# Optimization experiments

Measured on AMD Instinct MI355X. Metric: run time of the kernel, lower is better.

## Reference

```python
import jax, jax.numpy as jnp
import numpy as np

NUM_ITEMS = 50000
EMB = 16
SLATE = 10
HID = 512
LAT = 64
RESP = 1024
BATCH = 256


def _linear_params(k, out_dim, in_dim):
    kw, kb = jax.random.split(k)
    s = 1.0 / np.sqrt(in_dim)
    W = jax.random.uniform(kw, (out_dim, in_dim), jnp.float32, -s, s)
    b = jax.random.uniform(kb, (out_dim,), jnp.float32, -s, s)
    return W, b


def setup_inputs() -> dict:
    key = jax.random.key(0)
    ks = jax.random.split(key, 10)
    user_repr = jax.random.randint(ks[0], (BATCH, NUM_ITEMS), 0, 2, dtype=jnp.int32)
    slate = jax.random.randint(ks[1], (BATCH, SLATE), 0, NUM_ITEMS, dtype=jnp.int32)
    response_encoded = jax.random.uniform(ks[2], (BATCH, RESP), jnp.float32)
    eps = jax.random.normal(ks[3], (BATCH, LAT), jnp.float32)
    emb = jax.random.normal(ks[4], (NUM_ITEMS, EMB), jnp.float32)
    in_enc = SLATE * EMB + EMB + RESP
    W_enc, b_enc = _linear_params(ks[5], HID, in_enc)
    W_mu, b_mu = _linear_params(ks[6], LAT, HID)
    W_lv, b_lv = _linear_params(ks[7], LAT, HID)
    in_dec = LAT + EMB + RESP
    W_d1, b_d1 = _linear_params(ks[8], HID, in_dec)
    W_d2, b_d2 = _linear_params(ks[9], SLATE * EMB, HID)
    return {"user_repr": user_repr, "slate": slate, "response_encoded": response_encoded,
            "eps": eps, "emb": emb, "W_enc": W_enc, "b_enc": b_enc,
            "W_mu": W_mu, "b_mu": b_mu, "W_lv": W_lv, "b_lv": b_lv,
            "W_d1": W_d1, "b_d1": b_d1, "W_d2": W_d2, "b_d2": b_d2}


def reference(user_repr, slate, response_encoded, eps, emb,
              W_enc, b_enc, W_mu, b_mu, W_lv, b_lv, W_d1, b_d1, W_d2, b_d2):
    # Ragged embedding-mean pooling over interacted items (vectorized segment mean):
    # mean of emb rows where user_repr==1  ==  (indicator @ emb) / count
    uf = user_repr.astype(jnp.float32)                       # [B, N]
    counts = jnp.sum(uf, axis=1, keepdims=True)              # [B, 1]
    user = (uf @ emb) / counts                               # [B, E]

    cond = jnp.concatenate([user, response_encoded], axis=1)  # [B, E+R]
    slate_emb = emb[slate]                                    # [B, K, E]
    slate_vec = slate_emb.reshape(-1, SLATE * EMB)            # [B, K*E]
    x = jnp.concatenate([slate_vec, cond], axis=1)

    # encoder
    h = jax.nn.relu(x @ W_enc.T + b_enc)
    z_mean = h @ W_mu.T + b_mu
    z_log_var = h @ W_lv.T + b_lv

    # reparameterized sample
    z = z_mean + eps * jnp.exp(0.5 * z_log_var)

    # decoder
    dz = jnp.concatenate([z, cond], axis=1)
    dh = jax.nn.relu(dz @ W_d1.T + b_d1)
    rx = jax.nn.relu(dh @ W_d2.T + b_d2)                      # [B, K*E]
    rx = rx.reshape(-1, SLATE, EMB)                           # [B, K, E]

    # scores vs all items, softmax over items
    logits = jnp.einsum('bkh,nh->bkn', rx, emb)               # [B, K, N]
    probs = jax.nn.softmax(logits, axis=2)
    recon_slate = jnp.argmax(probs, axis=2)                   # [B, K]
    recon_resp = jnp.take_along_axis(probs, slate[:, :, None], axis=2)[..., 0]  # [B, K]
    return z_mean, z_log_var, recon_slate, recon_resp
```

## Files before the change

### kernel.cpp

```cpp
#include <hip/hip_runtime.h>

#define NITEMS 50000
#define EMBD   16
#define NSLATE 10
#define HIDD   512
#define LATD   64
#define RESPD  1024
#define BATCH  256
#define NCHUNK 8
#define CHUNK  6250
#define PCHUNK 3125
#define LOG2E  1.44269504088896340736f
#define SHIFT  64.0f

#define OUT_ZM 0
#define OUT_ZLV 16384
#define OUT_RS 32768
#define OUT_RR 35328

#define WS_X    0
#define WS_DZ   307200
#define WS_P2   0
#define WS_PP   589824
#define WS_PART 589824
#define WS_RX   1114112
#define WS_SPS  1155072
#define WS_SPM  1175552
#define WS_SPA  1196032

__global__ __launch_bounds__(256) void pool_part(const int* __restrict__ u,
    const float* __restrict__ emb, float* __restrict__ pp) {
  int b = blockIdx.x, c = blockIdx.y, t = threadIdx.x;
  float acc[16];
  #pragma unroll
  for (int i = 0; i < 16; ++i) acc[i] = 0.0f;
  float cnt = 0.0f;
  const int* ub = u + (size_t)b * NITEMS;
  int n1 = c * PCHUNK + PCHUNK;
  for (int n = c * PCHUNK + t; n < n1; n += 256) {
    if (ub[n]) {
      const float4* e4 = (const float4*)(emb + (size_t)n * 16);
      float4 a = e4[0], bb = e4[1], cc = e4[2], dd = e4[3];
      acc[0] += a.x;  acc[1] += a.y;  acc[2] += a.z;  acc[3] += a.w;
      acc[4] += bb.x; acc[5] += bb.y; acc[6] += bb.z; acc[7] += bb.w;
      acc[8] += cc.x; acc[9] += cc.y; acc[10] += cc.z; acc[11] += cc.w;
      acc[12] += dd.x; acc[13] += dd.y; acc[14] += dd.z; acc[15] += dd.w;
      cnt += 1.0f;
    }
  }
  #pragma unroll
  for (int off = 32; off > 0; off >>= 1) {
    #pragma unroll
    for (int i = 0; i < 16; ++i) acc[i] += __shfl_down(acc[i], off);
    cnt += __shfl_down(cnt, off);
  }
  int lane = t & 63, wv = t >> 6;
  if (lane == 0) {
    float* dst = pp + ((size_t)(b * 16 + c) * 4 + wv) * 17;
    #pragma unroll
    for (int i = 0; i < 16; ++i) dst[i] = acc[i];
    dst[16] = cnt;
  }
}

__global__ __launch_bounds__(256) void build_x(const float* __restrict__ pp,
    const int* __restrict__ slate, const float* __restrict__ resp,
    const float* __restrict__ emb, float* __restrict__ x, float* __restrict__ dz) {
  __shared__ float fin[17];
  int b = blockIdx.x, t = threadIdx.x;
  if (t < 17) {
    float a = 0.f;
    const float* p = pp + (size_t)b * 64 * 17 + t;
    #pragma unroll
    for (int w = 0; w < 64; ++w) a += p[w * 17];
    fin[t] = a;
  }
  __syncthreads();
  float inv = 1.0f / fin[16];
  if (t < 16) {
    float uv = fin[t] * inv;
    x[b * 1200 + 160 + t] = uv;
    dz[b * 1104 + 64 + t] = uv;
  }
  if (t >= 32 && t < 192) {
    int i = t - 32;
    int k = i >> 4, e = i & 15;
    int it = slate[b * 10 + k];
    x[b * 1200 + i] = emb[(size_t)it * 16 + e];
  }
  for (int i = t; i < 1024; i += 256) {
    float r = resp[b * 1024 + i];
    x[b * 1200 + 176 + i] = r;
    dz[b * 1104 + 80 + i] = r;
  }
}

__global__ __launch_bounds__(256) void gemm64(const float* __restrict__ A,
    const float* __restrict__ B, float* __restrict__ P, int M, int N, int K, int kChunk) {
  __shared__ float As[16][68];
  __shared__ float Bs[16][68];
  int tid = threadIdx.x;
  int m0 = blockIdx.y * 64, n0 = blockIdx.x * 64;
  int ks = blockIdx.z * kChunk;
  int ke = ks + kChunk; if (ke > K) ke = K;
  int sr = tid >> 2;
  int sc = (tid & 3) * 4;
  int tx = tid & 15, ty = tid >> 4;
  float acc[4][4];
  #pragma unroll
  for (int i = 0; i < 4; ++i)
    #pragma unroll
    for (int j = 0; j < 4; ++j) acc[i][j] = 0.f;
  for (int k0 = ks; k0 < ke; k0 += 16) {
    float4 av = make_float4(0.f, 0.f, 0.f, 0.f);
    float4 bv = make_float4(0.f, 0.f, 0.f, 0.f);
    if (k0 + sc < ke)
      av = *(const float4*)(A + (size_t)(m0 + sr) * K + k0 + sc);
    if (k0 + sc < ke && n0 + sr < N)
      bv = *(const float4*)(B + (size_t)(n0 + sr) * K + k0 + sc);
    __syncthreads();
    As[sc][sr] = av.x; As[sc + 1][sr] = av.y; As[sc + 2][sr] = av.z; As[sc + 3][sr] = av.w;
    Bs[sc][sr] = bv.x; Bs[sc + 1][sr] = bv.y; Bs[sc + 2][sr] = bv.z; Bs[sc + 3][sr] = bv.w;
    __syncthreads();
    #pragma unroll
    for (int kk = 0; kk < 16; ++kk) {
      float4 a4 = *(const float4*)&As[kk][4 * ty];
      float4 b4 = *(const float4*)&Bs[kk][4 * tx];
      float a[4] = {a4.x, a4.y, a4.z, a4.w};
      float b[4] = {b4.x, b4.y, b4.z, b4.w};
      #pragma unroll
      for (int i = 0; i < 4; ++i)
        #pragma unroll
        for (int j = 0; j < 4; ++j) acc[i][j] = fmaf(a[i], b[j], acc[i][j]);
    }
  }
  float* Pz = P + (size_t)blockIdx.z * M * N;
  #pragma unroll
  for (int i = 0; i < 4; ++i) {
    int m = m0 + 4 * ty + i, n = n0 + 4 * tx;
    if (n < N)
      *(float4*)(Pz + (size_t)m * N + n) = make_float4(acc[i][0], acc[i][1], acc[i][2], acc[i][3]);
  }
}

__global__ __launch_bounds__(128) void mulv_z_kernel(const float* __restrict__ part,
    const float* __restrict__ benc,
    const float* __restrict__ Wmu, const float* __restrict__ bmu,
    const float* __restrict__ Wlv, const float* __restrict__ blv,
    const float* __restrict__ eps, float* __restrict__ out, float* __restrict__ dz) {
  __shared__ __align__(16) float hs[512];
  __shared__ float zms[64], zlvs[64];
  int b = blockIdx.x, t = threadIdx.x;
  for (int i = t; i < 512; i += 128) {
    float a = benc[i];
    #pragma unroll
    for (int s = 0; s < 4; ++s) a += part[(size_t)s * 131072 + b * 512 + i];
    hs[i] = fmaxf(a, 0.f);
  }
  __syncthreads();
  const float* Wr = (t < 64) ? (Wmu + (size_t)t * 512) : (Wlv + (size_t)(t - 64) * 512);
  float bias = (t < 64) ? bmu[t] : blv[t - 64];
  const float4* w4 = (const float4*)Wr;
  const float4* h4 = (const float4*)hs;
  float a0 = 0.f, a1 = 0.f, a2 = 0.f, a3 = 0.f;
  #pragma unroll 4
  for (int i = 0; i < 128; ++i) {
    float4 w = w4[i], hv = h4[i];
    a0 = fmaf(w.x, hv.x, a0); a1 = fmaf(w.y, hv.y, a1);
    a2 = fmaf(w.z, hv.z, a2); a3 = fmaf(w.w, hv.w, a3);
  }
  float acc = (a0 + a1) + (a2 + a3) + bias;
  if (t < 64) { out[OUT_ZM + b * 64 + t] = acc; zms[t] = acc; }
  else        { out[OUT_ZLV + b * 64 + (t - 64)] = acc; zlvs[t - 64] = acc; }
  __syncthreads();
  if (t < 64) {
    float zv = fmaf(eps[b * 64 + t], __builtin_amdgcn_exp2f(0.7213475204444817f * zlvs[t]), zms[t]);
    dz[b * 1104 + t] = zv;
  }
}

__global__ __launch_bounds__(256) void gemm_d2(const float* __restrict__ part,
    const float* __restrict__ bd1, const float* __restrict__ W, float* __restrict__ p2) {
  __shared__ float As[16][68];
  __shared__ float Bs[16][68];
  const int N = 160;
  int tid = threadIdx.x;
  int m0 = blockIdx.y * 64, n0 = blockIdx.x * 64;
  int ks = blockIdx.z * 64, ke = ks + 64;
  int sr = tid >> 2, sc = (tid & 3) * 4;
  int tx = tid & 15, ty = tid >> 4;
  float acc[4][4];
  #pragma unroll
  for (int i = 0; i < 4; ++i)
    #pragma unroll
    for (int j = 0; j < 4; ++j) acc[i][j] = 0.f;
  for (int k0 = ks; k0 < ke; k0 += 16) {
    int col = k0 + sc;
    const float* p = part + (size_t)(m0 + sr) * 512 + col;
    float4 a0 = *(const float4*)(p);
    float4 a1 = *(const float4*)(p + 131072);
    float4 a2 = *(const float4*)(p + 262144);
    float4 a3 = *(const float4*)(p + 393216);
    float4 bb = *(const float4*)(bd1 + col);
    float4 av;
    av.x = fmaxf(a0.x + a1.x + a2.x + a3.x + bb.x, 0.f);
    av.y = fmaxf(a0.y + a1.y + a2.y + a3.y + bb.y, 0.f);
    av.z = fmaxf(a0.z + a1.z + a2.z + a3.z + bb.z, 0.f);
    av.w = fmaxf(a0.w + a1.w + a2.w + a3.w + bb.w, 0.f);
    float4 bv = make_float4(0.f, 0.f, 0.f, 0.f);
    if (n0 + sr < N)
      bv = *(const float4*)(W + (size_t)(n0 + sr) * 512 + col);
    __syncthreads();
    As[sc][sr] = av.x; As[sc + 1][sr] = av.y; As[sc + 2][sr] = av.z; As[sc + 3][sr] = av.w;
    Bs[sc][sr] = bv.x; Bs[sc + 1][sr] = bv.y; Bs[sc + 2][sr] = bv.z; Bs[sc + 3][sr] = bv.w;
    __syncthreads();
    #pragma unroll
    for (int kk = 0; kk < 16; ++kk) {
      float4 a4 = *(const float4*)&As[kk][4 * ty];
      float4 b4 = *(const float4*)&Bs[kk][4 * tx];
      float a[4] = {a4.x, a4.y, a4.z, a4.w};
      float b[4] = {b4.x, b4.y, b4.z, b4.w};
      #pragma unroll
      for (int i = 0; i < 4; ++i)
        #pragma unroll
        for (int j = 0; j < 4; ++j) acc[i][j] = fmaf(a[i], b[j], acc[i][j]);
    }
  }
  float* Pz = p2 + (size_t)blockIdx.z * 40960;
  #pragma unroll
  for (int i = 0; i < 4; ++i) {
    int m = m0 + 4 * ty + i, n = n0 + 4 * tx;
    if (n < N)
      *(float4*)(Pz + (size_t)m * 160 + n) = make_float4(acc[i][0], acc[i][1], acc[i][2], acc[i][3]);
  }
}

__global__ __launch_bounds__(256, 2) void score_part(const float* __restrict__ p2,
    const float* __restrict__ bd2, const float* __restrict__ emb,
    float* __restrict__ rx, float* __restrict__ psg, float* __restrict__ pmg,
    int* __restrict__ pag) {
  __shared__ __align__(16) float rxs[160];
  __shared__ float wm[4][10], wsum[4][10];
  __shared__ int wa[4][10];
  int b = blockIdx.x, c = blockIdx.y, t = threadIdx.x;
  if (t < 160) {
    float a = bd2[t];
    #pragma unroll
    for (int z = 0; z < 8; ++z) a += p2[(size_t)z * 40960 + b * 160 + t];
    float v = fmaxf(a, 0.f) * LOG2E;
    rxs[t] = v;
    if (c == 0) rx[b * 160 + t] = v;
  }
  __syncthreads();
  float m[10], s[10];
  int am[10];
  #pragma unroll
  for (int k = 0; k < 10; ++k) { m[k] = -3.402823466e38f; s[k] = 0.f; am[k] = 0; }
  int nBase = c * CHUNK;
  const float4* ep = (const float4*)emb;
  #pragma unroll 1
  for (int j = 0; j < 12; ++j) {
    int n0 = nBase + j * 512 + t;
    float4 e[2][4];
    #pragma unroll
    for (int it = 0; it < 2; ++it) {
      const float4* p = ep + (size_t)(n0 + it * 256) * 4;
      e[it][0] = p[0]; e[it][1] = p[1]; e[it][2] = p[2]; e[it][3] = p[3];
    }
    #pragma unroll
    for (int k = 0; k < 10; ++k) {
      float4 r0 = *(const float4*)(rxs + k * 16);
      float4 r1 = *(const float4*)(rxs + k * 16 + 4);
      float4 r2 = *(const float4*)(rxs + k * 16 + 8);
      float4 r3 = *(const float4*)(rxs + k * 16 + 12);
      #pragma unroll
      for (int it = 0; it < 2; ++it) {
        float x0 = fmaf(e[it][0].x, r0.x, -SHIFT);
        float x1 = e[it][1].x * r1.x;
        float x2 = e[it][2].x * r2.x;
        float x3 = e[it][3].x * r3.x;
        x0 = fmaf(e[it][0].y, r0.y, x0);
        x1 = fmaf(e[it][1].y, r1.y, x1);
        x2 = fmaf(e[it][2].y, r2.y, x2);
        x3 = fmaf(e[it][3].y, r3.y, x3);
        x0 = fmaf(e[it][0].z, r0.z, x0);
        x1 = fmaf(e[it][1].z, r1.z, x1);
        x2 = fmaf(e[it][2].z, r2.z, x2);
        x3 = fmaf(e[it][3].z, r3.z, x3);
        x0 = fmaf(e[it][0].w, r0.w, x0);
        x1 = fmaf(e[it][1].w, r1.w, x1);
        x2 = fmaf(e[it][2].w, r2.w, x2);
        x3 = fmaf(e[it][3].w, r3.w, x3);
        float x = (x0 + x1) + (x2 + x3);
        s[k] += __builtin_amdgcn_exp2f(x);
        if (x > m[k]) { m[k] = x; am[k] = n0 + it * 256; }
      }
    }
  }
  if (t < CHUNK - 6144) {
    int n = nBase + 6144 + t;
    const float4* p = ep + (size_t)n * 4;
    float4 e0 = p[0], e1 = p[1], e2 = p[2], e3 = p[3];
    #pragma unroll
    for (int k = 0; k < 10; ++k) {
      const float4 r0 = *(const float4*)(rxs + k * 16);
      const float4 r1 = *(const float4*)(rxs + k * 16 + 4);
      const float4 r2 = *(const float4*)(rxs + k * 16 + 8);
      const float4 r3 = *(const float4*)(rxs + k * 16 + 12);
      float x0 = fmaf(e0.w, r0.w, fmaf(e0.z, r0.z, fmaf(e0.y, r0.y, fmaf(e0.x, r0.x, -SHIFT))));
      float x1 = fmaf(e1.w, r1.w, fmaf(e1.z, r1.z, fmaf(e1.y, r1.y, e1.x * r1.x)));
      float x2 = fmaf(e2.w, r2.w, fmaf(e2.z, r2.z, fmaf(e2.y, r2.y, e2.x * r2.x)));
      float x3 = fmaf(e3.w, r3.w, fmaf(e3.z, r3.z, fmaf(e3.y, r3.y, e3.x * r3.x)));
      float x = (x0 + x1) + (x2 + x3);
      s[k] += __builtin_amdgcn_exp2f(x);
      if (x > m[k]) { m[k] = x; am[k] = n; }
    }
  }
  #pragma unroll
  for (int off = 32; off > 0; off >>= 1) {
    #pragma unroll
    for (int k = 0; k < 10; ++k) {
      s[k] += __shfl_down(s[k], off);
      float om = __shfl_down(m[k], off);
      int oa = __shfl_down(am[k], off);
      bool take = (om > m[k]) || (om == m[k] && oa < am[k]);
      am[k] = take ? oa : am[k];
      m[k] = fmaxf(m[k], om);
    }
  }
  int lane = t & 63, wv = t >> 6;
  if (lane == 0) {
    #pragma unroll
    for (int k = 0; k < 10; ++k) { wm[wv][k] = m[k]; wsum[wv][k] = s[k]; wa[wv][k] = am[k]; }
  }
  __syncthreads();
  if (t < 10) {
    int k = t;
    float M = wm[0][k], S = wsum[0][k];
    int AM = wa[0][k];
    #pragma unroll
    for (int w = 1; w < 4; ++w) {
      float m2 = wm[w][k];
      int oa = wa[w][k];
      bool take = (m2 > M) || (m2 == M && oa < AM);
      AM = take ? oa : AM;
      M = fmaxf(M, m2);
      S += wsum[w][k];
    }
    int idx = (b * NCHUNK + c) * 10 + k;
    psg[idx] = S; pmg[idx] = M; pag[idx] = AM;
  }
}

__global__ __launch_bounds__(256) void score_final(const float* __restrict__ psg,
    const float* __restrict__ pmg, const int* __restrict__ pag,
    const float* __restrict__ rx, const float* __restrict__ emb,
    const int* __restrict__ slate, float* __restrict__ out) {
  int tid = blockIdx.x * 256 + threadIdx.x;
  if (tid >= BATCH * 10) return;
  int b = tid / 10, k = tid % 10;
  int base = b * NCHUNK * 10 + k;
  float S = 0.f, M = -3.402823466e38f;
  int AM = 2147483647;
  #pragma unroll
  for (int c = 0; c < NCHUNK; ++c) {
    S += psg[base + c * 10];
    float m2 = pmg[base + c * 10];
    int oa = pag[base + c * 10];
    bool take = (m2 > M) || (m2 == M && oa < AM);
    AM = take ? oa : AM;
    M = fmaxf(M, m2);
  }
  int it = slate[b * 10 + k];
  const float* er = emb + (size_t)it * 16;
  const float* rr = rx + b * 160 + k * 16;
  float xs = -SHIFT;
  #pragma unroll
  for (int e = 0; e < 16; ++e) xs = fmaf(rr[e], er[e], xs);
  out[OUT_RS + b * 10 + k] = (float)AM;
  out[OUT_RR + b * 10 + k] = __builtin_amdgcn_exp2f(xs) / S;
}

extern "C" void kernel_launch(void* const* d_in, const int* in_sizes, int n_in,
                              void* d_out, int out_size, void* d_ws, size_t ws_size,
                              hipStream_t stream) {
  const int* user_repr = (const int*)d_in[0];
  const int* slate = (const int*)d_in[1];
  const float* resp = (const float*)d_in[2];
  const float* eps = (const float*)d_in[3];
  const float* emb = (const float*)d_in[4];
  const float* W_enc = (const float*)d_in[5];
  const float* b_enc = (const float*)d_in[6];
  const float* W_mu = (const float*)d_in[7];
  const float* b_mu = (const float*)d_in[8];
  const float* W_lv = (const float*)d_in[9];
  const float* b_lv = (const float*)d_in[10];
  const float* W_d1 = (const float*)d_in[11];
  const float* b_d1 = (const float*)d_in[12];
  const float* W_d2 = (const float*)d_in[13];
  const float* b_d2 = (const float*)d_in[14];
  float* out = (float*)d_out;
  float* ws = (float*)d_ws;

  float* x    = ws + WS_X;
  float* dz   = ws + WS_DZ;
  float* p2   = ws + WS_P2;
  float* pp   = ws + WS_PP;
  float* part = ws + WS_PART;
  float* rx   = ws + WS_RX;
  float* sps  = ws + WS_SPS;
  float* spm  = ws + WS_SPM;
  int*   spa  = (int*)(ws + WS_SPA);

  pool_part<<<dim3(256, 16), 256, 0, stream>>>(user_repr, emb, pp);
  build_x<<<256, 256, 0, stream>>>(pp, slate, resp, emb, x, dz);
  gemm64<<<dim3(8, 4, 4), 256, 0, stream>>>(x, W_enc, part, 256, 512, 1200, 300);
  mulv_z_kernel<<<256, 128, 0, stream>>>(part, b_enc, W_mu, b_mu, W_lv, b_lv, eps, out, dz);
  gemm64<<<dim3(8, 4, 4), 256, 0, stream>>>(dz, W_d1, part, 256, 512, 1104, 276);
  gemm_d2<<<dim3(3, 4, 8), 256, 0, stream>>>(part, b_d1, W_d2, p2);
  score_part<<<dim3(256, 8), 256, 0, stream>>>(p2, b_d2, emb, rx, sps, spm, spa);
  score_final<<<10, 256, 0, stream>>>(sps, spm, spa, rx, emb, slate, out);
}
```

Measured before the change: 323.5 us.

## Fuse d2 bias/ReLU into GEMM epilogue and prefetch embeddings in scoring loop

gemm_d2 no longer splits K into eight partial slices. It now runs the full K loop and applies bias, ReLU and the log2e scaling in its epilogue, writing rx directly. score_part then loads rx into registers instead of reducing partials through shared memory. The scoring loop is restructured to process one item per iteration with software prefetch of the next embedding row, which removes the tail branch. The gemm_d2 grid drops from 96 blocks to 12, so that GEMM loses parallelism, and score_part register pressure rises with 40 float4 values held in registers.

```diff
diff --git a/kernel.cpp b/kernel.cpp
--- a/kernel.cpp
+++ b/kernel.cpp
@@ -20,7 +20,6 @@
 
 #define WS_X    0
 #define WS_DZ   307200
-#define WS_P2   0
 #define WS_PP   589824
 #define WS_PART 589824
 #define WS_RX   1114112
@@ -180,13 +179,13 @@
 }
 
 __global__ __launch_bounds__(256) void gemm_d2(const float* __restrict__ part,
-    const float* __restrict__ bd1, const float* __restrict__ W, float* __restrict__ p2) {
+    const float* __restrict__ bd1, const float* __restrict__ W,
+    const float* __restrict__ bias, float* __restrict__ rx) {
   __shared__ float As[16][68];
   __shared__ float Bs[16][68];
-  const int N = 160;
+  const int N = 160, K = 512;
   int tid = threadIdx.x;
   int m0 = blockIdx.y * 64, n0 = blockIdx.x * 64;
-  int ks = blockIdx.z * 64, ke = ks + 64;
   int sr = tid >> 2, sc = (tid & 3) * 4;
   int tx = tid & 15, ty = tid >> 4;
   float acc[4][4];
@@ -194,7 +193,7 @@
   for (int i = 0; i < 4; ++i)
     #pragma unroll
     for (int j = 0; j < 4; ++j) acc[i][j] = 0.f;
-  for (int k0 = ks; k0 < ke; k0 += 16) {
+  for (int k0 = 0; k0 < K; k0 += 16) {
     int col = k0 + sc;
     const float* p = part + (size_t)(m0 + sr) * 512 + col;
     float4 a0 = *(const float4*)(p);
@@ -226,95 +225,75 @@
         for (int j = 0; j < 4; ++j) acc[i][j] = fmaf(a[i], b[j], acc[i][j]);
     }
   }
-  float* Pz = p2 + (size_t)blockIdx.z * 40960;
   #pragma unroll
   for (int i = 0; i < 4; ++i) {
     int m = m0 + 4 * ty + i, n = n0 + 4 * tx;
-    if (n < N)
-      *(float4*)(Pz + (size_t)m * 160 + n) = make_float4(acc[i][0], acc[i][1], acc[i][2], acc[i][3]);
-  }
-}
-
-__global__ __launch_bounds__(256, 2) void score_part(const float* __restrict__ p2,
-    const float* __restrict__ bd2, const float* __restrict__ emb,
-    float* __restrict__ rx, float* __restrict__ psg, float* __restrict__ pmg,
+    if (n < N) {
+      float4 v;
+      v.x = fmaxf(acc[i][0] + bias[n], 0.f) * LOG2E;
+      v.y = fmaxf(acc[i][1] + bias[n + 1], 0.f) * LOG2E;
+      v.z = fmaxf(acc[i][2] + bias[n + 2], 0.f) * LOG2E;
+      v.w = fmaxf(acc[i][3] + bias[n + 3], 0.f) * LOG2E;
+      *(float4*)(rx + (size_t)m * 160 + n) = v;
+    }
+  }
+}
+
+__global__ __launch_bounds__(256, 2) void score_part(const float* __restrict__ rx,
+    const float* __restrict__ emb, float* __restrict__ psg, float* __restrict__ pmg,
     int* __restrict__ pag) {
-  __shared__ __align__(16) float rxs[160];
   __shared__ float wm[4][10], wsum[4][10];
   __shared__ int wa[4][10];
   int b = blockIdx.x, c = blockIdx.y, t = threadIdx.x;
-  if (t < 160) {
-    float a = bd2[t];
-    #pragma unroll
-    for (int z = 0; z < 8; ++z) a += p2[(size_t)z * 40960 + b * 160 + t];
-    float v = fmaxf(a, 0.f) * LOG2E;
-    rxs[t] = v;
-    if (c == 0) rx[b * 160 + t] = v;
-  }
-  __syncthreads();
+  float4 r[10][4];
+  {
+    const float4* rp = (const float4*)(rx + b * 160);
+    #pragma unroll
+    for (int k = 0; k < 10; ++k) {
+      #pragma unroll
+      for (int j = 0; j < 4; ++j) r[k][j] = rp[k * 4 + j];
+    }
+  }
   float m[10], s[10];
   int am[10];
   #pragma unroll
   for (int k = 0; k < 10; ++k) { m[k] = -3.402823466e38f; s[k] = 0.f; am[k] = 0; }
-  int nBase = c * CHUNK;
+  int nBase = c * CHUNK, nEnd = nBase + CHUNK;
   const float4* ep = (const float4*)emb;
+  int n = nBase + t;
+  float4 e0, e1, e2, e3;
+  {
+    const float4* p = ep + (size_t)n * 4;
+    e0 = p[0]; e1 = p[1]; e2 = p[2]; e3 = p[3];
+  }
   #pragma unroll 1
-  for (int j = 0; j < 12; ++j) {
-    int n0 = nBase + j * 512 + t;
-    float4 e[2][4];
-    #pragma unroll
-    for (int it = 0; it < 2; ++it) {
-      const float4* p = ep + (size_t)(n0 + it * 256) * 4;
-      e[it][0] = p[0]; e[it][1] = p[1]; e[it][2] = p[2]; e[it][3] = p[3];
-    }
+  for (; n < nEnd; n += 256) {
+    int nn = n + 256; if (nn > NITEMS - 1) nn = NITEMS - 1;
+    const float4* p = ep + (size_t)nn * 4;
+    float4 f0 = p[0], f1 = p[1], f2 = p[2], f3 = p[3];
     #pragma unroll
     for (int k = 0; k < 10; ++k) {
-      float4 r0 = *(const float4*)(rxs + k * 16);
-      float4 r1 = *(const float4*)(rxs + k * 16 + 4);
-      float4 r2 = *(const float4*)(rxs + k * 16 + 8);
-      float4 r3 = *(const float4*)(rxs + k * 16 + 12);
-      #pragma unroll
-      for (int it = 0; it < 2; ++it) {
-        float x0 = fmaf(e[it][0].x, r0.x, -SHIFT);
-        float x1 = e[it][1].x * r1.x;
-        float x2 = e[it][2].x * r2.x;
-        float x3 = e[it][3].x * r3.x;
-        x0 = fmaf(e[it][0].y, r0.y, x0);
-        x1 = fmaf(e[it][1].y, r1.y, x1);
-        x2 = fmaf(e[it][2].y, r2.y, x2);
-        x3 = fmaf(e[it][3].y, r3.y, x3);
-        x0 = fmaf(e[it][0].z, r0.z, x0);
-        x1 = fmaf(e[it][1].z, r1.z, x1);
-        x2 = fmaf(e[it][2].z, r2.z, x2);
-        x3 = fmaf(e[it][3].z, r3.z, x3);
-        x0 = fmaf(e[it][0].w, r0.w, x0);
-        x1 = fmaf(e[it][1].w, r1.w, x1);
-        x2 = fmaf(e[it][2].w, r2.w, x2);
-        x3 = fmaf(e[it][3].w, r3.w, x3);
-        float x = (x0 + x1) + (x2 + x3);
-        s[k] += __builtin_amdgcn_exp2f(x);
-        if (x > m[k]) { m[k] = x; am[k] = n0 + it * 256; }
-      }
-    }
-  }
-  if (t < CHUNK - 6144) {
-    int n = nBase + 6144 + t;
-    const float4* p = ep + (size_t)n * 4;
-    float4 e0 = p[0], e1 = p[1], e2 = p[2], e3 = p[3];
-    #pragma unroll
-    for (int k = 0; k < 10; ++k) {
-      const float4 r0 = *(const float4*)(rxs + k * 16);
-      const float4 r1 = *(const float4*)(rxs + k * 16 + 4);
-      const float4 r2 = *(const float4*)(rxs + k * 16 + 8);
-      const float4 r3 = *(const float4*)(rxs + k * 16 + 12);
-      float x0 = fmaf(e0.w, r0.w, fmaf(e0.z, r0.z, fmaf(e0.y, r0.y, fmaf(e0.x, r0.x, -SHIFT))));
-      float x1 = fmaf(e1.w, r1.w, fmaf(e1.z, r1.z, fmaf(e1.y, r1.y, e1.x * r1.x)));
-      float x2 = fmaf(e2.w, r2.w, fmaf(e2.z, r2.z, fmaf(e2.y, r2.y, e2.x * r2.x)));
-      float x3 = fmaf(e3.w, r3.w, fmaf(e3.z, r3.z, fmaf(e3.y, r3.y, e3.x * r3.x)));
+      float x0 = fmaf(e0.x, r[k][0].x, -SHIFT);
+      float x1 = e1.x * r[k][1].x;
+      float x2 = e2.x * r[k][2].x;
+      float x3 = e3.x * r[k][3].x;
+      x0 = fmaf(e0.y, r[k][0].y, x0);
+      x1 = fmaf(e1.y, r[k][1].y, x1);
+      x2 = fmaf(e2.y, r[k][2].y, x2);
+      x3 = fmaf(e3.y, r[k][3].y, x3);
+      x0 = fmaf(e0.z, r[k][0].z, x0);
+      x1 = fmaf(e1.z, r[k][1].z, x1);
+      x2 = fmaf(e2.z, r[k][2].z, x2);
+      x3 = fmaf(e3.z, r[k][3].z, x3);
+      x0 = fmaf(e0.w, r[k][0].w, x0);
+      x1 = fmaf(e1.w, r[k][1].w, x1);
+      x2 = fmaf(e2.w, r[k][2].w, x2);
+      x3 = fmaf(e3.w, r[k][3].w, x3);
       float x = (x0 + x1) + (x2 + x3);
       s[k] += __builtin_amdgcn_exp2f(x);
       if (x > m[k]) { m[k] = x; am[k] = n; }
     }
+    e0 = f0; e1 = f1; e2 = f2; e3 = f3;
   }
   #pragma unroll
   for (int off = 32; off > 0; off >>= 1) {
@@ -404,7 +383,6 @@
 
   float* x    = ws + WS_X;
   float* dz   = ws + WS_DZ;
-  float* p2   = ws + WS_P2;
   float* pp   = ws + WS_PP;
   float* part = ws + WS_PART;
   float* rx   = ws + WS_RX;
@@ -417,7 +395,7 @@
   gemm64<<<dim3(8, 4, 4), 256, 0, stream>>>(x, W_enc, part, 256, 512, 1200, 300);
   mulv_z_kernel<<<256, 128, 0, stream>>>(part, b_enc, W_mu, b_mu, W_lv, b_lv, eps, out, dz);
   gemm64<<<dim3(8, 4, 4), 256, 0, stream>>>(dz, W_d1, part, 256, 512, 1104, 276);
-  gemm_d2<<<dim3(3, 4, 8), 256, 0, stream>>>(part, b_d1, W_d2, p2);
-  score_part<<<dim3(256, 8), 256, 0, stream>>>(p2, b_d2, emb, rx, sps, spm, spa);
+  gemm_d2<<<dim3(3, 4), 256, 0, stream>>>(part, b_d1, W_d2, b_d2, rx);
+  score_part<<<dim3(256, 8), 256, 0, stream>>>(rx, emb, sps, spm, spa);
   score_final<<<10, 256, 0, stream>>>(sps, spm, spa, rx, emb, slate, out);
 }
```

Result: slower. 352.5 us (+9.0%).

## Share staged embedding tiles across four batch rows in pooling kernel

Applied to the files above, without the earlier changes.

The pooling kernel now handles four batch rows per block. Each 256-item tile of the embedding table is staged once into padded shared memory and reused across all four rows, replacing per-row global gathers of embedding rows. This cuts redundant embedding reads and divergent gathers by a factor of four, but adds shared-memory staging, barriers and a larger register footprint (64 accumulators per thread). Grid size drops from 4096 to 1024 blocks.

```diff
diff --git a/kernel.cpp b/kernel.cpp
--- a/kernel.cpp
+++ b/kernel.cpp
@@ -10,6 +10,7 @@
 #define NCHUNK 8
 #define CHUNK  6250
 #define PCHUNK 3125
+#define PB     4
 #define LOG2E  1.44269504088896340736f
 #define SHIFT  64.0f
 
@@ -19,8 +20,8 @@
 #define OUT_RR 35328
 
 #define WS_X    0
+#define WS_P2   0
 #define WS_DZ   307200
-#define WS_P2   0
 #define WS_PP   589824
 #define WS_PART 589824
 #define WS_RX   1114112
@@ -30,36 +31,67 @@
 
 __global__ __launch_bounds__(256) void pool_part(const int* __restrict__ u,
     const float* __restrict__ emb, float* __restrict__ pp) {
-  int b = blockIdx.x, c = blockIdx.y, t = threadIdx.x;
-  float acc[16];
-  #pragma unroll
-  for (int i = 0; i < 16; ++i) acc[i] = 0.0f;
-  float cnt = 0.0f;
-  const int* ub = u + (size_t)b * NITEMS;
-  int n1 = c * PCHUNK + PCHUNK;
-  for (int n = c * PCHUNK + t; n < n1; n += 256) {
-    if (ub[n]) {
-      const float4* e4 = (const float4*)(emb + (size_t)n * 16);
-      float4 a = e4[0], bb = e4[1], cc = e4[2], dd = e4[3];
-      acc[0] += a.x;  acc[1] += a.y;  acc[2] += a.z;  acc[3] += a.w;
-      acc[4] += bb.x; acc[5] += bb.y; acc[6] += bb.z; acc[7] += bb.w;
-      acc[8] += cc.x; acc[9] += cc.y; acc[10] += cc.z; acc[11] += cc.w;
-      acc[12] += dd.x; acc[13] += dd.y; acc[14] += dd.z; acc[15] += dd.w;
-      cnt += 1.0f;
+  __shared__ float se[256 * 17];
+  int g = blockIdx.x, c = blockIdx.y, t = threadIdx.x;
+  int b0 = g * PB;
+  float acc[PB][16];
+  float cnt[PB];
+  #pragma unroll
+  for (int r = 0; r < PB; ++r) {
+    cnt[r] = 0.f;
+    #pragma unroll
+    for (int e = 0; e < 16; ++e) acc[r][e] = 0.f;
+  }
+  int base0 = c * PCHUNK;
+  const float4* emb4 = (const float4*)emb;
+  #pragma unroll 1
+  for (int st = 0; st < 13; ++st) {
+    int base = base0 + st * 256;
+    int tile = PCHUNK - st * 256; if (tile > 256) tile = 256;
+    int nf4 = tile * 4;
+    __syncthreads();
+    for (int v = t; v < nf4; v += 256) {
+      float4 f = emb4[(size_t)base * 4 + v];
+      int item = v >> 2, p = (v & 3) * 4;
+      se[item * 17 + p + 0] = f.x;
+      se[item * 17 + p + 1] = f.y;
+      se[item * 17 + p + 2] = f.z;
+      se[item * 17 + p + 3] = f.w;
+    }
+    __syncthreads();
+    if (t < tile) {
+      int n = base + t;
+      float ev[16];
+      #pragma unroll
+      for (int e = 0; e < 16; ++e) ev[e] = se[t * 17 + e];
+      #pragma unroll
+      for (int r = 0; r < PB; ++r) {
+        if (u[(size_t)(b0 + r) * NITEMS + n]) {
+          #pragma unroll
+          for (int e = 0; e < 16; ++e) acc[r][e] += ev[e];
+          cnt[r] += 1.f;
+        }
+      }
     }
   }
   #pragma unroll
   for (int off = 32; off > 0; off >>= 1) {
     #pragma unroll
-    for (int i = 0; i < 16; ++i) acc[i] += __shfl_down(acc[i], off);
-    cnt += __shfl_down(cnt, off);
+    for (int r = 0; r < PB; ++r) {
+      #pragma unroll
+      for (int e = 0; e < 16; ++e) acc[r][e] += __shfl_down(acc[r][e], off);
+      cnt[r] += __shfl_down(cnt[r], off);
+    }
   }
   int lane = t & 63, wv = t >> 6;
   if (lane == 0) {
-    float* dst = pp + ((size_t)(b * 16 + c) * 4 + wv) * 17;
-    #pragma unroll
-    for (int i = 0; i < 16; ++i) dst[i] = acc[i];
-    dst[16] = cnt;
+    #pragma unroll
+    for (int r = 0; r < PB; ++r) {
+      float* dst = pp + ((size_t)((b0 + r) * 16 + c) * 4 + wv) * 17;
+      #pragma unroll
+      for (int e = 0; e < 16; ++e) dst[e] = acc[r][e];
+      dst[16] = cnt[r];
+    }
   }
 }
 
@@ -103,8 +135,7 @@
   int m0 = blockIdx.y * 64, n0 = blockIdx.x * 64;
   int ks = blockIdx.z * kChunk;
   int ke = ks + kChunk; if (ke > K) ke = K;
-  int sr = tid >> 2;
-  int sc = (tid & 3) * 4;
+  int sr = tid >> 2, sc = (tid & 3) * 4;
   int tx = tid & 15, ty = tid >> 4;
   float acc[4][4];
   #pragma unroll
@@ -404,15 +435,15 @@
 
   float* x    = ws + WS_X;
   float* dz   = ws + WS_DZ;
-  float* p2   = ws + WS_P2;
   float* pp   = ws + WS_PP;
   float* part = ws + WS_PART;
+  float* p2   = ws + WS_P2;
   float* rx   = ws + WS_RX;
   float* sps  = ws + WS_SPS;
   float* spm  = ws + WS_SPM;
   int*   spa  = (int*)(ws + WS_SPA);
 
-  pool_part<<<dim3(256, 16), 256, 0, stream>>>(user_repr, emb, pp);
+  pool_part<<<dim3(64, 16), 256, 0, stream>>>(user_repr, emb, pp);
   build_x<<<256, 256, 0, stream>>>(pp, slate, resp, emb, x, dz);
   gemm64<<<dim3(8, 4, 4), 256, 0, stream>>>(x, W_enc, part, 256, 512, 1200, 300);
   mulv_z_kernel<<<256, 128, 0, stream>>>(part, b_enc, W_mu, b_mu, W_lv, b_lv, eps, out, dz);
```

After: 364.7 us. +12.8%, slower.
